# Kernel optimization log

Hardware: AMD Instinct MI355X
Metric: run time of the kernel (lower is better)

## Reference

```python
import jax, jax.numpy as jnp
import numpy as np

NEG_RATIO = 5          # neg_sample_ratio, also k (num_nodes-1 >> ratio)
THRESH = 0.7           # hard_neg_threshold
SMOOTH = 0.1           # label_smoothing
NUM_NODES = 200_000
DIM = 128
B = 1024               # batch size, all labels == 1 (all positives)
FILL_VAL = -1.0e9


def _l2_normalize(x, eps=1e-12):
    # F.normalize(p=2, dim=-1): divide by clamped L2 norm
    n = jnp.sqrt(jnp.sum(x * x, axis=-1, keepdims=True))
    return x / jnp.maximum(n, eps)


def setup_inputs() -> dict:
    key = jax.random.key(0)
    k1, k2, k3, k4 = jax.random.split(key, 4)
    src_nodes = jax.random.randint(k1, (B,), 0, NUM_NODES)
    dst_nodes = jax.random.randint(k2, (B,), 0, NUM_NODES)
    labels = jnp.ones((B,), dtype=jnp.float32)  # all positives -> pos_mask all True
    timestamps = jax.random.uniform(k3, (B,), dtype=jnp.float32)
    memory = jax.random.normal(k4, (NUM_NODES, DIM), dtype=jnp.float32)
    return {
        "src_nodes": src_nodes,
        "dst_nodes": dst_nodes,
        "labels": labels,
        "timestamps": timestamps,
        "memory": memory,
    }


def reference(src_nodes, dst_nodes, labels, timestamps, memory):
    # --- embedding gather + L2 normalize ---
    src_emb = memory[src_nodes]                      # [B, D]
    s = _l2_normalize(src_emb).astype(jnp.float16)   # use_half_precision=True
    c = _l2_normalize(memory).astype(jnp.float16)    # [N, D]

    # --- similarity [B, N], back to fp32 ---
    sim = jnp.matmul(s, c.T).astype(jnp.float32)

    # --- mask out ground-truth dst and below-threshold sims ---
    cols = jnp.arange(NUM_NODES)
    allowed = cols[None, :] != dst_nodes[:, None]    # exclude GT positives
    valid = allowed & (sim > THRESH)
    score = jnp.where(valid, sim, FILL_VAL)

    # --- top-k hard negatives per positive ---
    k = NEG_RATIO  # min(neg_sample_ratio, num_nodes-1)
    topk_vals, topk_idx = jax.lax.top_k(score, k)    # [B, k]
    is_real = (topk_vals > FILL_VAL + 1.0).reshape(-1)  # [B*k]

    # --- fallback random negatives (fixed-shape equivalent of the torch
    #     pack-real-then-pad-random assembly; total count == B*k either way) ---
    rkey = jax.random.key(42)
    rand_dst = jax.random.randint(rkey, (B * k,), 0, NUM_NODES)
    src_rep = jnp.repeat(src_nodes, k)               # [B*k]
    rand_dst = jnp.where(rand_dst == src_rep, (rand_dst + 1) % NUM_NODES, rand_dst)

    final_src = src_rep
    final_dst = jnp.where(is_real, topk_idx.reshape(-1), rand_dst)
    neg_ts = jnp.repeat(timestamps, k)

    # --- assemble augmented batch ---
    new_src = jnp.concatenate([src_nodes, final_src])
    new_dst = jnp.concatenate([dst_nodes, final_dst])
    new_labels = jnp.concatenate([labels, jnp.zeros((B * k,), labels.dtype)])
    new_ts = jnp.concatenate([timestamps, neg_ts])

    # --- label smoothing ---
    new_labels = new_labels * (1.0 - SMOOTH) + (1.0 - new_labels) * SMOOTH

    return new_src, new_dst, new_labels, new_ts, topk_vals
```

## Files before the change

kernel.cpp:

```cpp
#include <hip/hip_runtime.h>

#define NUM_NODES 200000
#define DIM 128
#define BATCH 1024
#define K_NEG 5
#define CAP 16
#define NBLK 250
#define CPB 800
#define TCOL 32
#define NT 25
#define THRESH 0.7f
#define FILL (-1.0e9f)

typedef __attribute__((ext_vector_type(8))) short short8;
typedef __attribute__((ext_vector_type(16))) float f32x16;

__device__ __forceinline__ unsigned short f2bf(float x) {
  unsigned u = __builtin_bit_cast(unsigned, x);
  return (unsigned short)((u + 0x7fffu + ((u >> 16) & 1u)) >> 16);
}

__device__ __forceinline__ void tf2x32(unsigned k0, unsigned k1,
                                       unsigned x0, unsigned x1,
                                       unsigned* o0, unsigned* o1) {
  unsigned ks2 = k0 ^ k1 ^ 0x1BD11BDAu;
  unsigned v0 = x0 + k0, v1 = x1 + k1;
#define TFR(r) { v0 += v1; v1 = (v1 << r) | (v1 >> (32 - r)); v1 ^= v0; }
  TFR(13) TFR(15) TFR(26) TFR(6)   v0 += k1;  v1 += ks2 + 1u;
  TFR(17) TFR(29) TFR(16) TFR(24)  v0 += ks2; v1 += k0 + 2u;
  TFR(13) TFR(15) TFR(26) TFR(6)   v0 += k0;  v1 += k1 + 3u;
  TFR(17) TFR(29) TFR(16) TFR(24)  v0 += k1;  v1 += ks2 + 4u;
  TFR(13) TFR(15) TFR(26) TFR(6)   v0 += ks2; v1 += k0 + 5u;
#undef TFR
  *o0 = v0; *o1 = v1;
}

__device__ __forceinline__ unsigned rbits32(unsigned ka, unsigned kb, unsigned m) {
  unsigned o0, o1;
  tf2x32(ka, kb, 0u, m, &o0, &o1);
  return o0 ^ o1;
}

__global__ void prep_kernel(const float* __restrict__ memory,
                            const int* __restrict__ src_nodes,
                            unsigned short* __restrict__ s16f,
                            int* __restrict__ cand_cnt) {
  int tid = threadIdx.x;
  int gid = blockIdx.x * 256 + tid;
  if (gid < BATCH) cand_cnt[gid] = 0;
  int row = blockIdx.x * 4 + (tid >> 6);
  int L = tid & 63;
  int s = src_nodes[row];
  float2 v = ((const float2*)(memory + (size_t)s * DIM))[L];
  float ss = v.x * v.x + v.y * v.y;
#pragma unroll
  for (int off = 32; off > 0; off >>= 1) ss += __shfl_xor(ss, off);
  float inv = 1.0f / fmaxf(sqrtf(ss), 1e-12f);
  unsigned p = (unsigned)f2bf(v.x * inv) | ((unsigned)f2bf(v.y * inv) << 16);
  int ms = row >> 5, l32 = row & 31;
  int c = L >> 2;
  int ks = c >> 1, half = c & 1;
  ((unsigned*)s16f)[(((ms * 8 + ks) * 64) + half * 32 + l32) * 4 + (L & 3)] = p;
}

__global__ __launch_bounds__(512, 2) void sim_scan_kernel(
    const float* __restrict__ memory,
    const unsigned short* __restrict__ s16f,
    const int* __restrict__ dst_nodes,
    int* __restrict__ cand_cnt,
    float* __restrict__ cand_val,
    int* __restrict__ cand_idx) {
  __shared__ unsigned short fragb[2][4096];
  __shared__ float nrmb[2][32];

  int tid = threadIdx.x;
  int wid = tid >> 6;
  int lane = tid & 63;
  int half = lane >> 5;
  int l32 = lane & 31;
  int jb0 = blockIdx.x * CPB;

  int ccol = wid * 4 + (lane & 3);
  int cseg = lane >> 2;

#define CONVERT(p, q0, q1) {                                                    \
    float ss = q0.x * q0.x + q0.y * q0.y + q0.z * q0.z + q0.w * q0.w            \
             + q1.x * q1.x + q1.y * q1.y + q1.z * q1.z + q1.w * q1.w;           \
    ss += __shfl_xor(ss, 4); ss += __shfl_xor(ss, 8);                           \
    ss += __shfl_xor(ss, 16); ss += __shfl_xor(ss, 32);                         \
    short8 f;                                                                   \
    f[0] = (short)f2bf(q0.x); f[1] = (short)f2bf(q0.y);                         \
    f[2] = (short)f2bf(q0.z); f[3] = (short)f2bf(q0.w);                         \
    f[4] = (short)f2bf(q1.x); f[5] = (short)f2bf(q1.y);                         \
    f[6] = (short)f2bf(q1.z); f[7] = (short)f2bf(q1.w);                         \
    *(short8*)((char*)fragb[p] + ((cseg * 32 + ccol) << 4)) = f;                \
    if (cseg == 0) nrmb[p][ccol] = fmaxf(sqrtf(ss), 1e-12f);                    \
  }

  float4 q0, q1;
  {
    const float4* rp4 = (const float4*)(memory + (size_t)(jb0 + ccol) * DIM);
    q0 = rp4[cseg * 2];
    q1 = rp4[cseg * 2 + 1];
  }
  const short8* __restrict__ af = (const short8*)s16f;
  short8 a[4][8];
#pragma unroll
  for (int m = 0; m < 4; ++m)
#pragma unroll
    for (int ks = 0; ks < 8; ++ks)
      a[m][ks] = af[(((wid * 4 + m) * 8) + ks) * 64 + lane];
  CONVERT(0, q0, q1);
  __syncthreads();

  f32x16 Z;
#pragma unroll
  for (int i = 0; i < 16; ++i) Z[i] = 0.0f;

  for (int t = 0; t < NT; ++t) {
    int par = t & 1;

    if (t + 1 < NT) {
      const float4* rp4 =
          (const float4*)(memory + (size_t)(jb0 + (t + 1) * TCOL + ccol) * DIM);
      q0 = rp4[cseg * 2];
      q1 = rp4[cseg * 2 + 1];
    }

    float nv = nrmb[par][l32];
    float thr = THRESH * nv;
    float invv = 1.0f / nv;
    int gj = jb0 + t * TCOL + l32;
    short8 bf[8];
#pragma unroll
    for (int ks = 0; ks < 8; ++ks)
      bf[ks] = *(const short8*)((char*)fragb[par] + (((2 * ks + half) * 32 + l32) << 4));

#pragma unroll
    for (int mp = 0; mp < 2; ++mp) {
      f32x16 accA = __builtin_amdgcn_mfma_f32_32x32x16_bf16(a[mp * 2][0], bf[0], Z, 0, 0, 0);
      f32x16 accB = __builtin_amdgcn_mfma_f32_32x32x16_bf16(a[mp * 2 + 1][0], bf[0], Z, 0, 0, 0);
#pragma unroll
      for (int ks = 1; ks < 8; ++ks) {
        accA = __builtin_amdgcn_mfma_f32_32x32x16_bf16(a[mp * 2][ks], bf[ks], accA, 0, 0, 0);
        accB = __builtin_amdgcn_mfma_f32_32x32x16_bf16(a[mp * 2 + 1][ks], bf[ks], accB, 0, 0, 0);
      }
      float mA = accA[0], mB = accB[0];
#pragma unroll
      for (int i = 1; i < 16; ++i) { mA = fmaxf(mA, accA[i]); mB = fmaxf(mB, accB[i]); }
      if (mA > thr || mB > thr) {
#pragma unroll
        for (int e = 0; e < 2; ++e) {
#pragma unroll
          for (int r = 0; r < 16; ++r) {
            float raw = (e == 0) ? accA[r] : accB[r];
            if (raw > thr) {
              int gi = (wid * 4 + mp * 2 + e) * 32 + (r & 3) + 8 * (r >> 2) + 4 * half;
              if (gj != dst_nodes[gi]) {
                int pq = atomicAdd(&cand_cnt[gi], 1);
                if (pq < CAP) {
                  cand_val[gi * CAP + pq] = raw * invv;
                  cand_idx[gi * CAP + pq] = gj;
                }
              }
            }
          }
        }
      }
    }

    if (t + 1 < NT) CONVERT(par ^ 1, q0, q1);

    __syncthreads();
  }
#undef CONVERT
}

__global__ void finalize_kernel(const int* __restrict__ src_nodes,
                                const int* __restrict__ dst_nodes,
                                const float* __restrict__ labels,
                                const float* __restrict__ ts,
                                const int* __restrict__ cand_cnt,
                                const float* __restrict__ cand_val,
                                const int* __restrict__ cand_idx,
                                float* __restrict__ out) {
  int r = blockIdx.x * 256 + threadIdx.x;
  if (r >= BATCH) return;
  const int TOT = BATCH + BATCH * K_NEG;
  int srcv = src_nodes[r];
  float tsv = ts[r];
  out[r] = (float)srcv;
  out[TOT + r] = (float)dst_nodes[r];
  float l = labels[r];
  out[2 * TOT + r] = l * 0.9f + (1.0f - l) * 0.1f;
  out[3 * TOT + r] = tsv;

  int cnt = cand_cnt[r];
  cnt = cnt < CAP ? cnt : CAP;
  float cv[CAP]; int ci[CAP];
  for (int i = 0; i < cnt; ++i) { cv[i] = cand_val[r * CAP + i]; ci[i] = cand_idx[r * CAP + i]; }

  unsigned k1a, k1b, k2a, k2b;
  tf2x32(0u, 42u, 0u, 0u, &k1a, &k1b);
  tf2x32(0u, 42u, 0u, 1u, &k2a, &k2b);

  const unsigned span = 200000u;
  const unsigned mult = 167296u;

  for (int s = 0; s < K_NEG; ++s) {
    int sel = -1;
    for (int i = 0; i < cnt; ++i)
      if (sel < 0 || cv[i] > cv[sel] || (cv[i] == cv[sel] && ci[i] < ci[sel])) sel = i;
    float v = FILL; int idx = 0;
    if (sel >= 0) { v = cv[sel]; idx = ci[sel]; cv[sel] = FILL; ci[sel] = 0x7fffffff; }
    bool is_real = v > (FILL + 1.0f);

    unsigned m = (unsigned)(r * K_NEG + s);
    unsigned hi = rbits32(k1a, k1b, m);
    unsigned lo = rbits32(k2a, k2b, m);
    unsigned off = ((hi % span) * mult + (lo % span)) % span;
    int rd = (int)off;
    if (rd == srcv) rd = (rd + 1) % NUM_NODES;
    int fd = is_real ? idx : rd;

    int mi = (int)m;
    out[BATCH + mi] = (float)srcv;
    out[TOT + BATCH + mi] = (float)fd;
    out[2 * TOT + BATCH + mi] = 0.1f;
    out[3 * TOT + BATCH + mi] = tsv;
    out[4 * TOT + mi] = v;
  }
}

extern "C" void kernel_launch(void* const* d_in, const int* in_sizes, int n_in,
                              void* d_out, int out_size, void* d_ws, size_t ws_size,
                              hipStream_t stream) {
  const int* src = (const int*)d_in[0];
  const int* dst = (const int*)d_in[1];
  const float* labels = (const float*)d_in[2];
  const float* ts = (const float*)d_in[3];
  const float* memory = (const float*)d_in[4];
  float* out = (float*)d_out;

  char* ws = (char*)d_ws;
  unsigned short* s16f = (unsigned short*)ws;
  int* cand_cnt = (int*)(ws + 262144);
  float* cand_val = (float*)(ws + 266240);
  int* cand_idx = (int*)(ws + 331776);

  prep_kernel<<<256, 256, 0, stream>>>(memory, src, s16f, cand_cnt);
  sim_scan_kernel<<<NBLK, 512, 0, stream>>>(memory, s16f, dst, cand_cnt, cand_val, cand_idx);
  finalize_kernel<<<(BATCH + 255) / 256, 256, 0, stream>>>(src, dst, labels, ts,
                                                           cand_cnt, cand_val, cand_idx, out);
}
```

Measured before the change: 188.3 us.

## Stage memory tiles via direct global-to-LDS loads and swizzle fragment buffer

The per-tile prefetch of node embeddings now uses global_load_lds to write straight into a per-wave LDS staging buffer, rather than holding the data in registers across the MFMA loop. Each wave then reads it back for normalization and bf16 conversion. The fragment buffer layout is also XOR-swizzled on both the write and read side to reduce LDS bank conflicts. This is meant to free VGPRs and lessen conflicts, at the cost of extra LDS traffic and a full vmcnt(0) wait before conversion.

```diff
diff --git a/kernel.cpp b/kernel.cpp
--- a/kernel.cpp
+++ b/kernel.cpp
@@ -18,6 +18,13 @@
 __device__ __forceinline__ unsigned short f2bf(float x) {
   unsigned u = __builtin_bit_cast(unsigned, x);
   return (unsigned short)((u + 0x7fffu + ((u >> 16) & 1u)) >> 16);
+}
+
+__device__ __forceinline__ void stage16(const void* g, void* l) {
+  __builtin_amdgcn_global_load_lds(
+      (const __attribute__((address_space(1))) unsigned int*)g,
+      (__attribute__((address_space(3))) unsigned int*)l,
+      16, 0, 0);
 }
 
 __device__ __forceinline__ void tf2x32(unsigned k0, unsigned k1,
@@ -70,6 +77,7 @@
     int* __restrict__ cand_cnt,
     float* __restrict__ cand_val,
     int* __restrict__ cand_idx) {
+  __shared__ char qbuf[8][2048];
   __shared__ unsigned short fragb[2][4096];
   __shared__ float nrmb[2][32];
 
@@ -83,7 +91,19 @@
   int ccol = wid * 4 + (lane & 3);
   int cseg = lane >> 2;
 
-#define CONVERT(p, q0, q1) {                                                    \
+  const char* mb = (const char*)memory;
+
+#define QSTAGE(t) {                                                             \
+    const char* g = mb + (size_t)(jb0 + (t) * TCOL + ccol) * 512 + (cseg << 5); \
+    stage16(g, &qbuf[wid][0]);                                                  \
+    stage16(g + 16, &qbuf[wid][1024]);                                          \
+  }
+
+#define QCONVERT(p) {                                                           \
+    asm volatile("s_waitcnt vmcnt(0)" ::: "memory");                            \
+    __builtin_amdgcn_sched_barrier(0);                                          \
+    float4 q0 = *(const float4*)(&qbuf[wid][lane << 4]);                        \
+    float4 q1 = *(const float4*)(&qbuf[wid][1024 + (lane << 4)]);               \
     float ss = q0.x * q0.x + q0.y * q0.y + q0.z * q0.z + q0.w * q0.w            \
              + q1.x * q1.x + q1.y * q1.y + q1.z * q1.z + q1.w * q1.w;           \
     ss += __shfl_xor(ss, 4); ss += __shfl_xor(ss, 8);                           \
@@ -93,16 +113,11 @@
     f[2] = (short)f2bf(q0.z); f[3] = (short)f2bf(q0.w);                         \
     f[4] = (short)f2bf(q1.x); f[5] = (short)f2bf(q1.y);                         \
     f[6] = (short)f2bf(q1.z); f[7] = (short)f2bf(q1.w);                         \
-    *(short8*)((char*)fragb[p] + ((cseg * 32 + ccol) << 4)) = f;                \
+    *(short8*)((char*)fragb[p] + ((cseg * 32 + (ccol ^ (cseg & 7))) << 4)) = f; \
     if (cseg == 0) nrmb[p][ccol] = fmaxf(sqrtf(ss), 1e-12f);                    \
   }
 
-  float4 q0, q1;
-  {
-    const float4* rp4 = (const float4*)(memory + (size_t)(jb0 + ccol) * DIM);
-    q0 = rp4[cseg * 2];
-    q1 = rp4[cseg * 2 + 1];
-  }
+  QSTAGE(0);
   const short8* __restrict__ af = (const short8*)s16f;
   short8 a[4][8];
 #pragma unroll
@@ -110,7 +125,7 @@
 #pragma unroll
     for (int ks = 0; ks < 8; ++ks)
       a[m][ks] = af[(((wid * 4 + m) * 8) + ks) * 64 + lane];
-  CONVERT(0, q0, q1);
+  QCONVERT(0);
   __syncthreads();
 
   f32x16 Z;
@@ -120,12 +135,7 @@
   for (int t = 0; t < NT; ++t) {
     int par = t & 1;
 
-    if (t + 1 < NT) {
-      const float4* rp4 =
-          (const float4*)(memory + (size_t)(jb0 + (t + 1) * TCOL + ccol) * DIM);
-      q0 = rp4[cseg * 2];
-      q1 = rp4[cseg * 2 + 1];
-    }
+    if (t + 1 < NT) QSTAGE(t + 1);
 
     float nv = nrmb[par][l32];
     float thr = THRESH * nv;
@@ -133,8 +143,10 @@
     int gj = jb0 + t * TCOL + l32;
     short8 bf[8];
 #pragma unroll
-    for (int ks = 0; ks < 8; ++ks)
-      bf[ks] = *(const short8*)((char*)fragb[par] + (((2 * ks + half) * 32 + l32) << 4));
+    for (int ks = 0; ks < 8; ++ks) {
+      int s0 = 2 * ks + half;
+      bf[ks] = *(const short8*)((char*)fragb[par] + ((s0 * 32 + (l32 ^ (s0 & 7))) << 4));
+    }
 
 #pragma unroll
     for (int mp = 0; mp < 2; ++mp) {
@@ -169,11 +181,12 @@
       }
     }
 
-    if (t + 1 < NT) CONVERT(par ^ 1, q0, q1);
+    if (t + 1 < NT) QCONVERT(par ^ 1);
 
     __syncthreads();
   }
-#undef CONVERT
+#undef QSTAGE
+#undef QCONVERT
 }
 
 __global__ void finalize_kernel(const int* __restrict__ src_nodes,
```

Result: faster. 183.4 us (-2.6%).

## Load candidate tiles directly into registers per wave, dropping shared-memory staging

Applied to the files above, without the earlier changes.

Before, one shared 32-column candidate tile was loaded cooperatively, converted to bf16 in LDS, double-buffered and synchronized with a barrier each step. Now every wave reads its own MFMA B fragments straight from global memory, converts them in registers and computes the column norm with one cross-half shuffle. This removes LDS traffic and block barriers. In exchange, all 8 waves in a block re-read and re-convert the same 32 columns (more L2/L1 traffic), and the software prefetch overlap of the next tile is gone.

```diff
diff --git a/kernel.cpp b/kernel.cpp
--- a/kernel.cpp
+++ b/kernel.cpp
@@ -6,9 +6,8 @@
 #define K_NEG 5
 #define CAP 16
 #define NBLK 250
-#define CPB 800
+#define NT 25
 #define TCOL 32
-#define NT 25
 #define THRESH 0.7f
 #define FILL (-1.0e9f)
 
@@ -70,39 +69,13 @@
     int* __restrict__ cand_cnt,
     float* __restrict__ cand_val,
     int* __restrict__ cand_idx) {
-  __shared__ unsigned short fragb[2][4096];
-  __shared__ float nrmb[2][32];
-
   int tid = threadIdx.x;
   int wid = tid >> 6;
   int lane = tid & 63;
-  int half = lane >> 5;
+  int fh = lane >> 5;
   int l32 = lane & 31;
-  int jb0 = blockIdx.x * CPB;
-
-  int ccol = wid * 4 + (lane & 3);
-  int cseg = lane >> 2;
-
-#define CONVERT(p, q0, q1) {                                                    \
-    float ss = q0.x * q0.x + q0.y * q0.y + q0.z * q0.z + q0.w * q0.w            \
-             + q1.x * q1.x + q1.y * q1.y + q1.z * q1.z + q1.w * q1.w;           \
-    ss += __shfl_xor(ss, 4); ss += __shfl_xor(ss, 8);                           \
-    ss += __shfl_xor(ss, 16); ss += __shfl_xor(ss, 32);                         \
-    short8 f;                                                                   \
-    f[0] = (short)f2bf(q0.x); f[1] = (short)f2bf(q0.y);                         \
-    f[2] = (short)f2bf(q0.z); f[3] = (short)f2bf(q0.w);                         \
-    f[4] = (short)f2bf(q1.x); f[5] = (short)f2bf(q1.y);                         \
-    f[6] = (short)f2bf(q1.z); f[7] = (short)f2bf(q1.w);                         \
-    *(short8*)((char*)fragb[p] + ((cseg * 32 + ccol) << 4)) = f;                \
-    if (cseg == 0) nrmb[p][ccol] = fmaxf(sqrtf(ss), 1e-12f);                    \
-  }
-
-  float4 q0, q1;
-  {
-    const float4* rp4 = (const float4*)(memory + (size_t)(jb0 + ccol) * DIM);
-    q0 = rp4[cseg * 2];
-    q1 = rp4[cseg * 2 + 1];
-  }
+  int tb = blockIdx.x * NT;
+
   const short8* __restrict__ af = (const short8*)s16f;
   short8 a[4][8];
 #pragma unroll
@@ -110,31 +83,35 @@
 #pragma unroll
     for (int ks = 0; ks < 8; ++ks)
       a[m][ks] = af[(((wid * 4 + m) * 8) + ks) * 64 + lane];
-  CONVERT(0, q0, q1);
-  __syncthreads();
 
   f32x16 Z;
 #pragma unroll
   for (int i = 0; i < 16; ++i) Z[i] = 0.0f;
 
   for (int t = 0; t < NT; ++t) {
-    int par = t & 1;
-
-    if (t + 1 < NT) {
-      const float4* rp4 =
-          (const float4*)(memory + (size_t)(jb0 + (t + 1) * TCOL + ccol) * DIM);
-      q0 = rp4[cseg * 2];
-      q1 = rp4[cseg * 2 + 1];
+    int jb = (tb + t) * TCOL;
+    int gj = jb + l32;
+
+    const float4* rp4 = (const float4*)(memory + (size_t)gj * DIM);
+    short8 bf[8];
+    float ss = 0.0f;
+#pragma unroll
+    for (int ks = 0; ks < 8; ++ks) {
+      float4 qa = rp4[ks * 4 + fh * 2];
+      float4 qb = rp4[ks * 4 + fh * 2 + 1];
+      ss += qa.x * qa.x + qa.y * qa.y + qa.z * qa.z + qa.w * qa.w;
+      ss += qb.x * qb.x + qb.y * qb.y + qb.z * qb.z + qb.w * qb.w;
+      short8 f;
+      f[0] = (short)f2bf(qa.x); f[1] = (short)f2bf(qa.y);
+      f[2] = (short)f2bf(qa.z); f[3] = (short)f2bf(qa.w);
+      f[4] = (short)f2bf(qb.x); f[5] = (short)f2bf(qb.y);
+      f[6] = (short)f2bf(qb.z); f[7] = (short)f2bf(qb.w);
+      bf[ks] = f;
     }
-
-    float nv = nrmb[par][l32];
-    float thr = THRESH * nv;
-    float invv = 1.0f / nv;
-    int gj = jb0 + t * TCOL + l32;
-    short8 bf[8];
-#pragma unroll
-    for (int ks = 0; ks < 8; ++ks)
-      bf[ks] = *(const short8*)((char*)fragb[par] + (((2 * ks + half) * 32 + l32) << 4));
+    ss += __shfl_xor(ss, 32);
+    float nrm = fmaxf(sqrtf(ss), 1e-12f);
+    float invv = 1.0f / nrm;
+    float thr = THRESH * nrm;
 
 #pragma unroll
     for (int mp = 0; mp < 2; ++mp) {
@@ -155,7 +132,7 @@
           for (int r = 0; r < 16; ++r) {
             float raw = (e == 0) ? accA[r] : accB[r];
             if (raw > thr) {
-              int gi = (wid * 4 + mp * 2 + e) * 32 + (r & 3) + 8 * (r >> 2) + 4 * half;
+              int gi = (wid * 4 + mp * 2 + e) * 32 + (r & 3) + 8 * (r >> 2) + 4 * fh;
               if (gj != dst_nodes[gi]) {
                 int pq = atomicAdd(&cand_cnt[gi], 1);
                 if (pq < CAP) {
@@ -168,12 +145,7 @@
         }
       }
     }
-
-    if (t + 1 < NT) CONVERT(par ^ 1, q0, q1);
-
-    __syncthreads();
   }
-#undef CONVERT
 }
 
 __global__ void finalize_kernel(const int* __restrict__ src_nodes,
```

After: 265.8 us. 41.2% more time.
